# Kernel tuning notes

Hardware: AMD Instinct MI355X
Metric: run time of the kernel (lower is better)

Reference implementation:

```python
import jax, jax.numpy as jnp
import numpy as np

D = 64
N = 262144


def _stack_four(A, B, C, Dm):
    return jnp.block([[A, B], [C, Dm]])


def setup_inputs() -> dict:
    key = jax.random.key(0)
    # Z: (2d+1, n+1) in-context prompt matrix
    Z = jax.random.normal(key, (2 * D + 1, N + 1), dtype=jnp.float32)
    # P: zeros with P[-1,-1] = 1 (selects last row)
    P = jnp.zeros((2 * D + 1, 2 * D + 1), dtype=jnp.float32).at[-1, -1].set(1.0)
    # Q: block matrix built from M1, M2, B as in TFLayer.__init__
    I = jnp.eye(D, dtype=jnp.float32)
    O = jnp.zeros((D, D), dtype=jnp.float32)
    M1 = _stack_four(-I, I, O, O)
    M2 = -M1
    Bm = _stack_four(I, O, O, O)  # C = eye(d), so C.T = I
    A = M2.T @ Bm @ M1            # (2d, 2d)
    Q = jnp.zeros((2 * D + 1, 2 * D + 1), dtype=jnp.float32).at[: 2 * D, : 2 * D].set(A)
    return {"Z": Z, "P": P, "Q": Q}


def reference(Z, P, Q):
    # next_Z = Z + (1/n) * P @ Z @ M @ Z.T @ Q @ Z
    # M = eye(n+1) with M[-1,-1] = 0, i.e. right-mult by M zeroes the last
    # column. We never materialize the (n+1, n+1) identity.
    n = Z.shape[1] - 1
    PZ = P @ Z                         # (2d+1, n+1)
    PZM = PZ.at[:, -1].set(0.0)        # apply M: zero last column
    S = PZM @ Z.T                      # (2d+1, 2d+1) -- the only big contraction
    upd = (S @ Q) @ Z                  # (2d+1, n+1)
    return Z + upd / n
```

## Files before the change

### kernel.cpp

```cpp
#include <hip/hip_runtime.h>

#define DD      64
#define ROWS    129
#define NCOLS   262145
#define NDOT    262144
#define DOTROWS 128
#define CHUNK   2048
#define NCHUNK  128

__global__ __launch_bounds__(256) void k_dot_copy(const float* __restrict__ Z,
                                                  float* __restrict__ out,
                                                  float* __restrict__ partials) {
    const int row   = blockIdx.x & (DOTROWS - 1);
    const int chunk = blockIdx.x >> 7;
    const long base = (long)chunk * CHUNK;
    const float* zr = Z + (long)row * NCOLS + base;
    const float* zl = Z + (long)DOTROWS * NCOLS + base;
    float* orow     = out + (long)row * NCOLS + base;
    const int tid = threadIdx.x;

    __shared__ float szl[CHUNK];
    const float4* zl4 = (const float4*)zl;
#pragma unroll
    for (int k = 0; k < CHUNK / 4 / 256; ++k) {
        ((float4*)szl)[tid + k * 256] = zl4[tid + k * 256];
    }
    __syncthreads();

    float acc = 0.f;
#pragma unroll
    for (int k = 0; k < CHUNK / 256; ++k) {
        const int c = tid + k * 256;
        const float v = zr[c];
        __builtin_nontemporal_store(v, &orow[c]);
        acc = fmaf(v, szl[c], acc);
    }
    if (chunk == NCHUNK - 1 && tid == 255) {
        __builtin_nontemporal_store(Z[(long)row * NCOLS + NDOT],
                                    &out[(long)row * NCOLS + NDOT]);
    }

#pragma unroll
    for (int off = 32; off; off >>= 1) acc += __shfl_down(acc, off, 64);
    __shared__ float s[4];
    if ((tid & 63) == 0) s[tid >> 6] = acc;
    __syncthreads();
    if (tid == 0) {
        partials[(long)row * NCHUNK + chunk] = s[0] + s[1] + s[2] + s[3];
    }
}

__global__ __launch_bounds__(256) void k_matvec(const float* __restrict__ partials,
                                                const float* __restrict__ Q,
                                                float* __restrict__ t) {
    const int j   = blockIdx.x;
    const int tid = threadIdx.x;
    float acc = 0.f;
#pragma unroll
    for (int k = 0; k < (DOTROWS * NCHUNK) / 256; ++k) {
        const int idx = tid + k * 256;
        const int m   = idx >> 7;
        acc = fmaf(partials[idx], Q[m * ROWS + j], acc);
    }
#pragma unroll
    for (int off = 32; off; off >>= 1) acc += __shfl_down(acc, off, 64);
    __shared__ float s[4];
    if ((tid & 63) == 0) s[tid >> 6] = acc;
    __syncthreads();
    if (tid == 0) t[j] = (s[0] + s[1] + s[2] + s[3]) * (1.0f / (float)NDOT);
}

__global__ __launch_bounds__(256) void k_row128(const float* __restrict__ Z,
                                               const float* __restrict__ t,
                                               float* __restrict__ out) {
    __shared__ float ts[DOTROWS];
    const int tid = threadIdx.x;
    if (tid < DOTROWS) ts[tid] = t[tid];
    __syncthreads();

    const long c = (long)blockIdx.x * 256 + tid;
    if (c >= NCOLS) return;

    const float* zp = Z + c;
    float acc = 0.f;
#pragma unroll 8
    for (int j = 0; j < DOTROWS; ++j) {
        acc = fmaf(ts[j], zp[(long)j * NCOLS], acc);
    }
    out[(long)DOTROWS * NCOLS + c] = Z[(long)DOTROWS * NCOLS + c] + acc;
}

extern "C" void kernel_launch(void* const* d_in, const int* in_sizes, int n_in,
                              void* d_out, int out_size, void* d_ws, size_t ws_size,
                              hipStream_t stream) {
    const float* Z = (const float*)d_in[0];
    const float* Q = (const float*)d_in[2];
    float* out = (float*)d_out;

    float* partials = (float*)d_ws;
    float* t        = partials + DOTROWS * NCHUNK;

    k_dot_copy<<<DOTROWS * NCHUNK, 256, 0, stream>>>(Z, out, partials);
    k_matvec<<<DOTROWS, 256, 0, stream>>>(partials, Q, t);
    k_row128<<<(NCOLS + 255) / 256, 256, 0, stream>>>(Z, t, out);
}
```

Measured before the change: 276.0 us.

## Vectorize row loads/stores with per-row alignment shift and padded LDS

Each row starts at a different 16-byte alignment because NCOLS is odd, so the dot/copy kernel now shifts by a per-row offset to issue aligned float4 loads and nontemporal stores, handling the few leftover elements as scalars. The last row is staged into padded shared memory to avoid bank conflicts on the strided reads, and the chunk size doubles so there are half as many partials. The row-128 kernel splits its accumulator four ways to expose more independent loads. This adds branch and indexing complexity plus changed summation order.

```diff
diff --git a/kernel.cpp b/kernel.cpp
--- a/kernel.cpp
+++ b/kernel.cpp
@@ -5,8 +5,12 @@
 #define NCOLS   262145
 #define NDOT    262144
 #define DOTROWS 128
-#define CHUNK   2048
-#define NCHUNK  128
+#define CHUNK   4096
+#define NCHUNK  64
+
+typedef float f32x4 __attribute__((ext_vector_type(4)));
+
+#define SIDX(i) ((i) + ((i) >> 2))
 
 __global__ __launch_bounds__(256) void k_dot_copy(const float* __restrict__ Z,
                                                   float* __restrict__ out,
@@ -14,39 +18,72 @@
     const int row   = blockIdx.x & (DOTROWS - 1);
     const int chunk = blockIdx.x >> 7;
     const long base = (long)chunk * CHUNK;
-    const float* zr = Z + (long)row * NCOLS + base;
+    const long roff = (long)row * NCOLS + base;
+    const float* zr = Z + roff;
+    float*       orow = out + roff;
     const float* zl = Z + (long)DOTROWS * NCOLS + base;
-    float* orow     = out + (long)row * NCOLS + base;
+
     const int tid = threadIdx.x;
+    __shared__ float szl[CHUNK + CHUNK / 4];
 
-    __shared__ float szl[CHUNK];
-    const float4* zl4 = (const float4*)zl;
+    {
+        const f32x4* zl4 = (const f32x4*)zl;
 #pragma unroll
-    for (int k = 0; k < CHUNK / 4 / 256; ++k) {
-        ((float4*)szl)[tid + k * 256] = zl4[tid + k * 256];
+        for (int k = 0; k < CHUNK / 4 / 256; ++k) {
+            const int j = tid + k * 256;
+            const f32x4 v = zl4[j];
+            szl[5 * j + 0] = v.x;
+            szl[5 * j + 1] = v.y;
+            szl[5 * j + 2] = v.z;
+            szl[5 * j + 3] = v.w;
+        }
     }
     __syncthreads();
 
+    const int s  = (4 - (row & 3)) & 3;
+    const int nq = (s == 0) ? CHUNK / 4 : CHUNK / 4 - 1;
+    const f32x4* zr4 = (const f32x4*)(zr + s);
+    f32x4*       o4  = (f32x4*)(orow + s);
+
     float acc = 0.f;
 #pragma unroll
-    for (int k = 0; k < CHUNK / 256; ++k) {
-        const int c = tid + k * 256;
-        const float v = zr[c];
-        __builtin_nontemporal_store(v, &orow[c]);
-        acc = fmaf(v, szl[c], acc);
+    for (int k = 0; k < CHUNK / 4 / 256; ++k) {
+        const int q = tid + k * 256;
+        if (q < nq) {
+            const f32x4 v = zr4[q];
+            __builtin_nontemporal_store(v, &o4[q]);
+            const int c = s + 4 * q;
+            acc = fmaf(v.x, szl[SIDX(c + 0)], acc);
+            acc = fmaf(v.y, szl[SIDX(c + 1)], acc);
+            acc = fmaf(v.z, szl[SIDX(c + 2)], acc);
+            acc = fmaf(v.w, szl[SIDX(c + 3)], acc);
+        }
     }
-    if (chunk == NCHUNK - 1 && tid == 255) {
+    if (s != 0) {
+        if (tid < s) {
+            const int c = tid;
+            const float v = zr[c];
+            __builtin_nontemporal_store(v, &orow[c]);
+            acc = fmaf(v, szl[SIDX(c)], acc);
+        } else if (tid >= 256 - (4 - s)) {
+            const int c = CHUNK - (256 - tid);
+            const float v = zr[c];
+            __builtin_nontemporal_store(v, &orow[c]);
+            acc = fmaf(v, szl[SIDX(c)], acc);
+        }
+    }
+    if (chunk == NCHUNK - 1 && tid == 128) {
         __builtin_nontemporal_store(Z[(long)row * NCOLS + NDOT],
                                     &out[(long)row * NCOLS + NDOT]);
     }
 
 #pragma unroll
     for (int off = 32; off; off >>= 1) acc += __shfl_down(acc, off, 64);
-    __shared__ float s[4];
-    if ((tid & 63) == 0) s[tid >> 6] = acc;
+    __syncthreads();
+    if ((tid & 63) == 0) szl[tid >> 6] = acc;
     __syncthreads();
     if (tid == 0) {
-        partials[(long)row * NCHUNK + chunk] = s[0] + s[1] + s[2] + s[3];
+        partials[(long)row * NCHUNK + chunk] = szl[0] + szl[1] + szl[2] + szl[3];
     }
 }
 
@@ -59,7 +96,7 @@
 #pragma unroll
     for (int k = 0; k < (DOTROWS * NCHUNK) / 256; ++k) {
         const int idx = tid + k * 256;
-        const int m   = idx >> 7;
+        const int m   = idx >> 6;
         acc = fmaf(partials[idx], Q[m * ROWS + j], acc);
     }
 #pragma unroll
@@ -82,12 +119,16 @@
     if (c >= NCOLS) return;
 
     const float* zp = Z + c;
-    float acc = 0.f;
+    float a0 = 0.f, a1 = 0.f, a2 = 0.f, a3 = 0.f;
 #pragma unroll 8
-    for (int j = 0; j < DOTROWS; ++j) {
-        acc = fmaf(ts[j], zp[(long)j * NCOLS], acc);
+    for (int j = 0; j < DOTROWS; j += 4) {
+        a0 = fmaf(ts[j + 0], zp[(long)(j + 0) * NCOLS], a0);
+        a1 = fmaf(ts[j + 1], zp[(long)(j + 1) * NCOLS], a1);
+        a2 = fmaf(ts[j + 2], zp[(long)(j + 2) * NCOLS], a2);
+        a3 = fmaf(ts[j + 3], zp[(long)(j + 3) * NCOLS], a3);
     }
-    out[(long)DOTROWS * NCOLS + c] = Z[(long)DOTROWS * NCOLS + c] + acc;
+    out[(long)DOTROWS * NCOLS + c] =
+        Z[(long)DOTROWS * NCOLS + c] + ((a0 + a1) + (a2 + a3));
 }
 
 extern "C" void kernel_launch(void* const* d_in, const int* in_sizes, int n_in,
```

After: 269.8 us. 2.2% less time.
